# Performance work log

Hardware: AMD Instinct MI355X
Metric: run time of the kernel (lower is better)

The kernel has to match this reference:

```python
import jax, jax.numpy as jnp
import numpy as np

ALPHA = 0.2  # LeakyReLU negative slope
NEG_INF = jnp.float32(-9e15)


def setup_inputs() -> dict:
    key = jax.random.key(0)
    k1, k2, k3, k4, k5, k6 = jax.random.split(key, 6)
    B, N, F_in, F_out = 8, 2048, 256, 64
    h = jax.random.normal(k1, (B, N, F_in), dtype=jnp.float32)
    adj = jax.random.randint(k2, (B, N, N), 0, 2, dtype=jnp.int32)
    level = jax.random.uniform(k3, (B, N), dtype=jnp.float32)
    node_type = jax.random.uniform(k4, (B, N, N), dtype=jnp.float32)
    W = jax.random.normal(k5, (F_in, F_out), dtype=jnp.float32) * 1.414 / np.sqrt(F_in)
    a = jax.random.normal(k6, (2 * F_out, 1), dtype=jnp.float32) * 1.414 / np.sqrt(2 * F_out)
    return {"h": h, "adj": adj, "level": level, "node_type": node_type, "W": W, "a": a}


def reference(h, adj, level, node_type, W, a):
    # h: [B,N,Fin], adj/node_type: [B,N,N], level: [B,N], W: [Fin,Fout], a: [2*Fout,1]
    F_out = W.shape[1]
    Wh = jnp.einsum('bnf,fo->bno', h, W)  # [B,N,Fout]
    # Additive attention decomposed: e[b,i,j] = a1.Wh_i + a2.Wh_j (no O(N^2*2F) tensor)
    a1 = a[:F_out, 0]
    a2 = a[F_out:, 0]
    f1 = Wh @ a1  # [B,N]
    f2 = Wh @ a2  # [B,N]
    e = jax.nn.leaky_relu(f1[:, :, None] + f2[:, None, :], negative_slope=ALPHA)  # [B,N,N]
    # gat_our=True path: node_type scales scores, level scales Wh
    e = e * node_type
    Wh = Wh * level[:, :, None]
    attention = jnp.where(adj > 0, e, NEG_INF)
    attention = jax.nn.softmax(attention, axis=1)  # faithful: original softmax over dim=1
    # dropout p=0 / eval mode -> identity
    h_prime = jnp.einsum('bij,bjo->bio', attention, Wh)  # [B,N,Fout]
    return jax.nn.relu(h_prime)  # concat=True
```

## Files before the change

kernel.cpp:

```cpp
#include <hip/hip_runtime.h>

#define BB 8
#define NN 2048
#define FIN 256
#define FO 64

typedef short short8_t __attribute__((ext_vector_type(8)));
typedef float float4_t __attribute__((ext_vector_type(4)));

__device__ __forceinline__ unsigned short f2bf(float x) {
  unsigned int u = __float_as_uint(x);
  unsigned int r = (u + 0x7fffu + ((u >> 16) & 1u)) >> 16;
  return (unsigned short)r;
}

#define GLD16(gp, lp)                                                          \
  __builtin_amdgcn_global_load_lds(                                            \
      (const __attribute__((address_space(1))) void*)(gp),                     \
      (__attribute__((address_space(3))) void*)(lp), 16, 0, 0)

__global__ __launch_bounds__(256) void k1_gemm(
    const float* __restrict__ h,
    const float* __restrict__ level,
    const float* __restrict__ W,
    const float* __restrict__ a,
    float* __restrict__ V, float* __restrict__ f1, float* __restrict__ f2,
    float* __restrict__ scol)
{
  __shared__ float wlds[128 * 64];
  __shared__ float hs[16 * 260];
  __shared__ float parts1[16 * 17];
  __shared__ float parts2[16 * 17];
  int t = threadIdx.x;
  int b = blockIdx.x >> 7;
  int i0 = (blockIdx.x & 127) * 16;

  if (blockIdx.x < 64) scol[blockIdx.x * 256 + t] = 0.0f;

  {
    int r_ld = t >> 4, f0 = (t & 15) * 16;
    const float* hp = h + (size_t)(b * NN + i0 + r_ld) * FIN + f0;
    float4 x0 = *(const float4*)(hp);
    float4 x1 = *(const float4*)(hp + 4);
    float4 x2 = *(const float4*)(hp + 8);
    float4 x3 = *(const float4*)(hp + 12);
    float* hd = &hs[r_ld * 260 + f0];
    *(float4*)(hd + 0) = x0; *(float4*)(hd + 4) = x1;
    *(float4*)(hd + 8) = x2; *(float4*)(hd + 12) = x3;
  }

  int r = t >> 4;
  int c4 = (t & 15) * 4;
  float4 acc = {0, 0, 0, 0};

  #pragma unroll
  for (int half = 0; half < 2; ++half) {
    __syncthreads();
    #pragma unroll
    for (int q = 0; q < 8; ++q) {
      int idx = q * 1024 + t * 4;
      *(float4*)&wlds[idx] = *(const float4*)&W[half * 8192 + idx];
    }
    __syncthreads();
    for (int f = 0; f < 128; f += 8) {
      float4 hv0 = *(const float4*)&hs[r * 260 + half * 128 + f];
      float4 hv1 = *(const float4*)&hs[r * 260 + half * 128 + f + 4];
      float hvv[8] = {hv0.x, hv0.y, hv0.z, hv0.w, hv1.x, hv1.y, hv1.z, hv1.w};
      #pragma unroll
      for (int k = 0; k < 8; ++k) {
        float4 wv = *(const float4*)&wlds[(f + k) * 64 + c4];
        acc.x += hvv[k] * wv.x; acc.y += hvv[k] * wv.y;
        acc.z += hvv[k] * wv.z; acc.w += hvv[k] * wv.w;
      }
    }
  }

  float p1 = acc.x * a[c4] + acc.y * a[c4 + 1] + acc.z * a[c4 + 2] + acc.w * a[c4 + 3];
  float p2 = acc.x * a[64 + c4] + acc.y * a[64 + c4 + 1] +
             acc.z * a[64 + c4 + 2] + acc.w * a[64 + c4 + 3];
  parts1[r * 17 + (t & 15)] = p1;
  parts2[r * 17 + (t & 15)] = p2;
  __syncthreads();
  if (t < 16) {
    float s1 = 0.f, s2 = 0.f;
    #pragma unroll
    for (int g = 0; g < 16; ++g) { s1 += parts1[t * 17 + g]; s2 += parts2[t * 17 + g]; }
    f1[b * NN + i0 + t] = s1;
    f2[b * NN + i0 + t] = s2;
  }

  float lv = level[b * NN + i0 + r];
  float4 vv = {acc.x * lv, acc.y * lv, acc.z * lv, acc.w * lv};
  *(float4*)&V[(size_t)(b * NN + i0 + r) * FO + c4] = vv;
}

__global__ __launch_bounds__(512) void k2a_stream(
    const int* __restrict__ adj,
    const float* __restrict__ ntp,
    const float* __restrict__ f1,
    const float* __restrict__ f2,
    unsigned short* __restrict__ u_bf,
    float* __restrict__ scol)
{
  int t = threadIdx.x;
  int b = blockIdx.x >> 7;
  int row0 = (blockIdx.x & 127) * 16;
  size_t base = (size_t)b * NN;
  int j0 = t * 4;

  float4 f2v = *(const float4*)(f2 + base + j0);
  float acc0 = 0.f, acc1 = 0.f, acc2 = 0.f, acc3 = 0.f;

  size_t rb = (base + row0) * (size_t)NN + j0;
  const int* ap = adj + rb;
  const float* np = ntp + rb;
  unsigned short* up = u_bf + rb;
  const float* f1p = f1 + base + row0;

  #pragma unroll 4
  for (int r = 0; r < 16; ++r) {
    int4 a4 = *(const int4*)(ap + (size_t)r * NN);
    float4 n4 = *(const float4*)(np + (size_t)r * NN);
    float f1v = f1p[r];
    float x0 = f1v + f2v.x; x0 = fmaxf(x0, 0.2f * x0);
    float x1 = f1v + f2v.y; x1 = fmaxf(x1, 0.2f * x1);
    float x2 = f1v + f2v.z; x2 = fmaxf(x2, 0.2f * x2);
    float x3 = f1v + f2v.w; x3 = fmaxf(x3, 0.2f * x3);
    float u0 = (a4.x > 0) ? __expf(x0 * n4.x) : 0.0f;
    float u1 = (a4.y > 0) ? __expf(x1 * n4.y) : 0.0f;
    float u2 = (a4.z > 0) ? __expf(x2 * n4.z) : 0.0f;
    float u3 = (a4.w > 0) ? __expf(x3 * n4.w) : 0.0f;
    acc0 += u0; acc1 += u1; acc2 += u2; acc3 += u3;
    unsigned int p0 = (unsigned int)f2bf(u0) | ((unsigned int)f2bf(u1) << 16);
    unsigned int p1 = (unsigned int)f2bf(u2) | ((unsigned int)f2bf(u3) << 16);
    *(uint2*)(up + (size_t)r * NN) = make_uint2(p0, p1);
  }

  atomicAdd(&scol[base + j0 + 0], acc0);
  atomicAdd(&scol[base + j0 + 1], acc1);
  atomicAdd(&scol[base + j0 + 2], acc2);
  atomicAdd(&scol[base + j0 + 3], acc3);
}

template <int STORE_U>
__global__ __launch_bounds__(512) void k2a_stats(
    const int* __restrict__ adj,
    const float* __restrict__ ntp,
    const float* __restrict__ f1,
    const float* __restrict__ f2,
    unsigned short* __restrict__ u_bf,
    unsigned char* __restrict__ bits,
    float* __restrict__ scol)
{
  __shared__ int ladj[2][16 * 256];
  __shared__ float lnt[2][16 * 256];
  __shared__ float red[2048];
  int t = threadIdx.x;
  int b = blockIdx.x >> 6;
  int row0 = (blockIdx.x & 63) * 32;
  int w = t >> 6, l = t & 63;
  size_t base = (size_t)b * NN;

  auto stage = [&](int buf, int s) {
    int tile = s >> 3, c = s & 7;
    int r0 = row0 + tile * 16 + 2 * w;
    const int* ga = adj + (base + r0) * NN + c * 256 + l * 4;
    const float* gn = ntp + (base + r0) * NN + c * 256 + l * 4;
    GLD16(ga, &ladj[buf][(2 * w) * 256]);
    GLD16(ga + NN, &ladj[buf][(2 * w + 1) * 256]);
    GLD16(gn, &lnt[buf][(2 * w) * 256]);
    GLD16(gn + NN, &lnt[buf][(2 * w + 1) * 256]);
  };

  int jj = t & 255;
  int rh = t >> 8;

  float accJ[8];
  #pragma unroll
  for (int c = 0; c < 8; ++c) accJ[c] = 0.f;
  float f2v[8];
  #pragma unroll
  for (int c = 0; c < 8; ++c) f2v[c] = f2[base + c * 256 + jj];

  stage(0, 0);
  for (int s = 0; s < 16; ++s) {
    int buf = s & 1;
    __syncthreads();
    if (s < 15) stage(buf ^ 1, s + 1);
    int tile = s >> 3, c = s & 7;
    #pragma unroll
    for (int q = 0; q < 8; ++q) {
      int r = rh * 8 + q;
      int av = ladj[buf][r * 256 + jj];
      float nv = lnt[buf][r * 256 + jj];
      float f1v = f1[base + row0 + tile * 16 + r];
      float x = f1v + f2v[c];
      x = fmaxf(x, 0.2f * x);
      bool m = av > 0;
      float u = m ? __expf(x * nv) : 0.0f;
      accJ[c] += u;
      if (STORE_U) {
        u_bf[(base + row0 + tile * 16 + r) * NN + c * 256 + jj] = f2bf(u);
      } else {
        unsigned long long bal = __ballot(m);
        if (l == 0)
          *(unsigned long long*)&bits[(base + row0 + tile * 16 + r) * (NN / 8)
                                      + c * 32 + (w & 3) * 8] = bal;
      }
    }
  }

  if (rh == 0) {
    #pragma unroll
    for (int c = 0; c < 8; ++c) red[c * 256 + jj] = accJ[c];
  }
  __syncthreads();
  if (rh == 1) {
    #pragma unroll
    for (int c = 0; c < 8; ++c) red[c * 256 + jj] += accJ[c];
  }
  __syncthreads();
  #pragma unroll
  for (int q = 0; q < 4; ++q)
    atomicAdd(&scol[base + q * 512 + t], red[q * 512 + t]);
}

__global__ __launch_bounds__(256) void k2b_pack(
    const float* __restrict__ V,
    const float* __restrict__ scol,
    unsigned short* __restrict__ vf)
{
  int t = threadIdx.x;
  int b = blockIdx.x >> 6;
  int kk = blockIdx.x & 63;
  int ng = t >> 6;
  int l = t & 63;
  int jb = kk * 32 + ((l >> 4) * 8);
  int o = ng * 16 + (l & 15);
  unsigned int pk[4];
  #pragma unroll
  for (int p = 0; p < 4; ++p) {
    int jr0 = jb + 2 * p, jr1 = jb + 2 * p + 1;
    float s0 = scol[b * NN + jr0];
    float s1 = scol[b * NN + jr1];
    float i0 = (s0 > 0.f) ? (1.0f / s0) : 0.0f;
    float i1 = (s1 > 0.f) ? (1.0f / s1) : 0.0f;
    float v0 = V[(size_t)(b * NN + jr0) * FO + o] * i0;
    float v1 = V[(size_t)(b * NN + jr1) * FO + o] * i1;
    pk[p] = (unsigned int)f2bf(v0) | ((unsigned int)f2bf(v1) << 16);
  }
  *(uint4*)(vf + (size_t)(((b * 64 + kk) * 4 + ng) * 64 + l) * 8) =
      make_uint4(pk[0], pk[1], pk[2], pk[3]);
}

__global__ __launch_bounds__(512, 4) void k3_agg_u3(
    const unsigned short* __restrict__ u_bf,
    const unsigned short* __restrict__ vf,
    float* __restrict__ outp)
{
  __shared__ float red[8 * 16 * 68];
  int t = threadIdx.x;
  int b = blockIdx.x >> 6;
  int tt = blockIdx.x & 63;
  int i0 = tt * 32;
  int w = t >> 6, l = t & 63;
  int col = l & 15, quad = l >> 4;
  const unsigned short* urow0 = u_bf + (size_t)(b * NN + i0 + col) * NN + quad * 8;
  const unsigned short* urow1 = urow0 + (size_t)16 * NN;
  const unsigned short* vbase = vf + (size_t)(b * 64) * 2048 + l * 8;

  float4_t acc[2][4];
  #pragma unroll
  for (int sgi = 0; sgi < 2; ++sgi)
    #pragma unroll
    for (int g = 0; g < 4; ++g) acc[sgi][g] = (float4_t){0, 0, 0, 0};

  int kk0 = w * 8;
  short8_t A0 = *(const short8_t*)(urow0 + kk0 * 32);
  short8_t A1 = *(const short8_t*)(urow1 + kk0 * 32);
  const unsigned short* vb0 = vbase + (size_t)kk0 * 2048;
  short8_t c0 = *(const short8_t*)(vb0);
  short8_t c1 = *(const short8_t*)(vb0 + 512);
  short8_t c2 = *(const short8_t*)(vb0 + 1024);
  short8_t c3 = *(const short8_t*)(vb0 + 1536);

  #pragma unroll
  for (int s = 0; s < 8; ++s) {
    short8_t nA0, nA1, n0, n1, n2, n3;
    if (s < 7) {
      int kk = w * 8 + s + 1;
      nA0 = *(const short8_t*)(urow0 + kk * 32);
      nA1 = *(const short8_t*)(urow1 + kk * 32);
      const unsigned short* vn = vbase + (size_t)kk * 2048;
      n0 = *(const short8_t*)(vn);
      n1 = *(const short8_t*)(vn + 512);
      n2 = *(const short8_t*)(vn + 1024);
      n3 = *(const short8_t*)(vn + 1536);
    }
    acc[0][0] = __builtin_amdgcn_mfma_f32_16x16x32_bf16(A0, c0, acc[0][0], 0, 0, 0);
    acc[0][1] = __builtin_amdgcn_mfma_f32_16x16x32_bf16(A0, c1, acc[0][1], 0, 0, 0);
    acc[0][2] = __builtin_amdgcn_mfma_f32_16x16x32_bf16(A0, c2, acc[0][2], 0, 0, 0);
    acc[0][3] = __builtin_amdgcn_mfma_f32_16x16x32_bf16(A0, c3, acc[0][3], 0, 0, 0);
    acc[1][0] = __builtin_amdgcn_mfma_f32_16x16x32_bf16(A1, c0, acc[1][0], 0, 0, 0);
    acc[1][1] = __builtin_amdgcn_mfma_f32_16x16x32_bf16(A1, c1, acc[1][1], 0, 0, 0);
    acc[1][2] = __builtin_amdgcn_mfma_f32_16x16x32_bf16(A1, c2, acc[1][2], 0, 0, 0);
    acc[1][3] = __builtin_amdgcn_mfma_f32_16x16x32_bf16(A1, c3, acc[1][3], 0, 0, 0);
    if (s < 7) { A0 = nA0; A1 = nA1; c0 = n0; c1 = n1; c2 = n2; c3 = n3; }
  }

  #pragma unroll
  for (int sub = 0; sub < 2; ++sub) {
    __syncthreads();
    #pragma unroll
    for (int r = 0; r < 4; ++r) {
      int rowi = quad * 4 + r;
      float* rp = &red[w * 1088 + rowi * 68 + col];
      rp[0] = acc[sub][0][r];
      rp[16] = acc[sub][1][r];
      rp[32] = acc[sub][2][r];
      rp[48] = acc[sub][3][r];
    }
    __syncthreads();
    if (t < 256) {
      int row = t >> 4, o4 = (t & 15) * 4;
      const float* rp = &red[row * 68 + o4];
      float4 s0 = *(const float4*)(rp);
      float4 s1 = *(const float4*)(rp + 1088);
      float4 s2 = *(const float4*)(rp + 2176);
      float4 s3 = *(const float4*)(rp + 3264);
      float4 s4 = *(const float4*)(rp + 4352);
      float4 s5 = *(const float4*)(rp + 5440);
      float4 s6 = *(const float4*)(rp + 6528);
      float4 s7 = *(const float4*)(rp + 7616);
      float4 o;
      o.x = fmaxf(s0.x + s1.x + s2.x + s3.x + s4.x + s5.x + s6.x + s7.x, 0.0f);
      o.y = fmaxf(s0.y + s1.y + s2.y + s3.y + s4.y + s5.y + s6.y + s7.y, 0.0f);
      o.z = fmaxf(s0.z + s1.z + s2.z + s3.z + s4.z + s5.z + s6.z + s7.z, 0.0f);
      o.w = fmaxf(s0.w + s1.w + s2.w + s3.w + s4.w + s5.w + s6.w + s7.w, 0.0f);
      *(float4*)&outp[(size_t)(b * NN + i0 + sub * 16 + row) * FO + o4] = o;
    }
  }
}

__global__ __launch_bounds__(256) void k3_agg_b(
    const float* __restrict__ ntp,
    const unsigned char* __restrict__ bits,
    const float* __restrict__ f1,
    const float* __restrict__ f2,
    const unsigned short* __restrict__ vf,
    float* __restrict__ outp)
{
  __shared__ float red[4 * 16 * 68];
  int t = threadIdx.x;
  int b = blockIdx.x >> 7;
  int i0 = (blockIdx.x & 127) * 16;
  int w = t >> 6, l = t & 63;
  int col = l & 15, quad = l >> 4;
  int gi = b * NN + i0 + col;
  float f1v = f1[gi];
  const float* ntrow = ntp + (size_t)gi * NN;
  const unsigned char* brow = bits + (size_t)gi * (NN / 8);
  float4_t acc0 = {0, 0, 0, 0}, acc1 = {0, 0, 0, 0}, acc2 = {0, 0, 0, 0}, acc3 = {0, 0, 0, 0};

  for (int s = 0; s < 16; ++s) {
    int kk = w * 16 + s;
    int jq = kk * 32 + quad * 8;
    unsigned int m8 = brow[jq >> 3];
    float4 n0 = *(const float4*)(ntrow + jq);
    float4 n1 = *(const float4*)(ntrow + jq + 4);
    float4 g0 = *(const float4*)(f2 + b * NN + jq);
    float4 g1 = *(const float4*)(f2 + b * NN + jq + 4);
    float f2v[8] = {g0.x, g0.y, g0.z, g0.w, g1.x, g1.y, g1.z, g1.w};
    float ntf[8] = {n0.x, n0.y, n0.z, n0.w, n1.x, n1.y, n1.z, n1.w};
    union { unsigned int u[4]; short8_t v; } A;
    #pragma unroll
    for (int p = 0; p < 4; ++p) {
      int e0 = 2 * p, e1 = 2 * p + 1;
      float x0 = f1v + f2v[e0]; x0 = fmaxf(x0, 0.2f * x0);
      float u0 = ((m8 >> e0) & 1u) ? __expf(x0 * ntf[e0]) : 0.0f;
      float x1 = f1v + f2v[e1]; x1 = fmaxf(x1, 0.2f * x1);
      float u1 = ((m8 >> e1) & 1u) ? __expf(x1 * ntf[e1]) : 0.0f;
      A.u[p] = (unsigned int)f2bf(u0) | ((unsigned int)f2bf(u1) << 16);
    }
    const unsigned short* vb = vf + (size_t)(b * 64 + kk) * 2048 + l * 8;
    short8_t bf0 = *(const short8_t*)(vb);
    short8_t bf1 = *(const short8_t*)(vb + 512);
    short8_t bf2 = *(const short8_t*)(vb + 1024);
    short8_t bf3 = *(const short8_t*)(vb + 1536);
    acc0 = __builtin_amdgcn_mfma_f32_16x16x32_bf16(A.v, bf0, acc0, 0, 0, 0);
    acc1 = __builtin_amdgcn_mfma_f32_16x16x32_bf16(A.v, bf1, acc1, 0, 0, 0);
    acc2 = __builtin_amdgcn_mfma_f32_16x16x32_bf16(A.v, bf2, acc2, 0, 0, 0);
    acc3 = __builtin_amdgcn_mfma_f32_16x16x32_bf16(A.v, bf3, acc3, 0, 0, 0);
  }

  #pragma unroll
  for (int r = 0; r < 4; ++r) {
    int rowi = quad * 4 + r;
    red[w * 1088 + rowi * 68 + 0 + col] = acc0[r];
    red[w * 1088 + rowi * 68 + 16 + col] = acc1[r];
    red[w * 1088 + rowi * 68 + 32 + col] = acc2[r];
    red[w * 1088 + rowi * 68 + 48 + col] = acc3[r];
  }
  __syncthreads();

  int row = t >> 4, o4 = (t & 15) * 4;
  const float* rp = &red[row * 68 + o4];
  float4 s0 = *(const float4*)(rp);
  float4 s1 = *(const float4*)(rp + 1088);
  float4 s2 = *(const float4*)(rp + 2176);
  float4 s3 = *(const float4*)(rp + 3264);
  float4 o;
  o.x = fmaxf(s0.x + s1.x + s2.x + s3.x, 0.0f);
  o.y = fmaxf(s0.y + s1.y + s2.y + s3.y, 0.0f);
  o.z = fmaxf(s0.z + s1.z + s2.z + s3.z, 0.0f);
  o.w = fmaxf(s0.w + s1.w + s2.w + s3.w, 0.0f);
  *(float4*)&outp[(size_t)(b * NN + i0 + row) * FO + o4] = o;
}

extern "C" void kernel_launch(void* const* d_in, const int* in_sizes, int n_in,
                              void* d_out, int out_size, void* d_ws, size_t ws_size,
                              hipStream_t stream) {
  const float* h = (const float*)d_in[0];
  const int* adj = (const int*)d_in[1];
  const float* level = (const float*)d_in[2];
  const float* ntm = (const float*)d_in[3];
  const float* W = (const float*)d_in[4];
  const float* a = (const float*)d_in[5];
  float* outp = (float*)d_out;

  float* V = (float*)d_ws;
  float* f1 = V + (size_t)BB * NN * FO;
  float* f2 = f1 + BB * NN;
  float* scol = f2 + BB * NN;
  unsigned short* vf = (unsigned short*)(scol + BB * NN);
  char* tail = (char*)(vf + (size_t)BB * NN * FO);
  size_t fixed = (size_t)(tail - (char*)d_ws);
  size_t need_u = fixed + (size_t)BB * NN * NN * 2;
  bool big = (ws_size >= need_u);

  k1_gemm<<<1024, 256, 0, stream>>>(h, level, W, a, V, f1, f2, scol);
  if (big) {
    unsigned short* u_bf = (unsigned short*)tail;
    k2a_stream<<<1024, 512, 0, stream>>>(adj, ntm, f1, f2, u_bf, scol);
    k2b_pack<<<512, 256, 0, stream>>>(V, scol, vf);
    k3_agg_u3<<<512, 512, 0, stream>>>(u_bf, vf, outp);
  } else {
    unsigned char* bits = (unsigned char*)tail;
    k2a_stats<0><<<512, 512, 0, stream>>>(adj, ntm, f1, f2, nullptr, bits, scol);
    k2b_pack<<<512, 256, 0, stream>>>(V, scol, vf);
    k3_agg_b<<<1024, 256, 0, stream>>>(ntm, bits, f1, f2, vf, outp);
  }
}
```

Before: 350.6 us.

## Replace column-sum atomics with per-rowblock partials and batch loads in stream kernel

```diff
diff --git a/kernel.cpp b/kernel.cpp
--- a/kernel.cpp
+++ b/kernel.cpp
@@ -100,11 +100,12 @@
     const float* __restrict__ f1,
     const float* __restrict__ f2,
     unsigned short* __restrict__ u_bf,
-    float* __restrict__ scol)
-{
-  int t = threadIdx.x;
-  int b = blockIdx.x >> 7;
-  int row0 = (blockIdx.x & 127) * 16;
+    float* __restrict__ partials)
+{
+  int t = threadIdx.x;
+  int b = blockIdx.x >> 6;
+  int rowblk = blockIdx.x & 63;
+  int row0 = rowblk * 32;
   size_t base = (size_t)b * NN;
   int j0 = t * 4;
 
@@ -117,29 +118,35 @@
   unsigned short* up = u_bf + rb;
   const float* f1p = f1 + base + row0;
 
-  #pragma unroll 4
-  for (int r = 0; r < 16; ++r) {
-    int4 a4 = *(const int4*)(ap + (size_t)r * NN);
-    float4 n4 = *(const float4*)(np + (size_t)r * NN);
-    float f1v = f1p[r];
-    float x0 = f1v + f2v.x; x0 = fmaxf(x0, 0.2f * x0);
-    float x1 = f1v + f2v.y; x1 = fmaxf(x1, 0.2f * x1);
-    float x2 = f1v + f2v.z; x2 = fmaxf(x2, 0.2f * x2);
-    float x3 = f1v + f2v.w; x3 = fmaxf(x3, 0.2f * x3);
-    float u0 = (a4.x > 0) ? __expf(x0 * n4.x) : 0.0f;
-    float u1 = (a4.y > 0) ? __expf(x1 * n4.y) : 0.0f;
-    float u2 = (a4.z > 0) ? __expf(x2 * n4.z) : 0.0f;
-    float u3 = (a4.w > 0) ? __expf(x3 * n4.w) : 0.0f;
-    acc0 += u0; acc1 += u1; acc2 += u2; acc3 += u3;
-    unsigned int p0 = (unsigned int)f2bf(u0) | ((unsigned int)f2bf(u1) << 16);
-    unsigned int p1 = (unsigned int)f2bf(u2) | ((unsigned int)f2bf(u3) << 16);
-    *(uint2*)(up + (size_t)r * NN) = make_uint2(p0, p1);
-  }
-
-  atomicAdd(&scol[base + j0 + 0], acc0);
-  atomicAdd(&scol[base + j0 + 1], acc1);
-  atomicAdd(&scol[base + j0 + 2], acc2);
-  atomicAdd(&scol[base + j0 + 3], acc3);
+  #pragma unroll
+  for (int g = 0; g < 4; ++g) {
+    int4 av[8];
+    float4 nv[8];
+    #pragma unroll
+    for (int rr = 0; rr < 8; ++rr) {
+      av[rr] = *(const int4*)(ap + (size_t)(g * 8 + rr) * NN);
+      nv[rr] = *(const float4*)(np + (size_t)(g * 8 + rr) * NN);
+    }
+    #pragma unroll
+    for (int rr = 0; rr < 8; ++rr) {
+      float f1v = f1p[g * 8 + rr];
+      float x0 = f1v + f2v.x; x0 = fmaxf(x0, 0.2f * x0);
+      float x1 = f1v + f2v.y; x1 = fmaxf(x1, 0.2f * x1);
+      float x2 = f1v + f2v.z; x2 = fmaxf(x2, 0.2f * x2);
+      float x3 = f1v + f2v.w; x3 = fmaxf(x3, 0.2f * x3);
+      float u0 = (av[rr].x > 0) ? __expf(x0 * nv[rr].x) : 0.0f;
+      float u1 = (av[rr].y > 0) ? __expf(x1 * nv[rr].y) : 0.0f;
+      float u2 = (av[rr].z > 0) ? __expf(x2 * nv[rr].z) : 0.0f;
+      float u3 = (av[rr].w > 0) ? __expf(x3 * nv[rr].w) : 0.0f;
+      acc0 += u0; acc1 += u1; acc2 += u2; acc3 += u3;
+      unsigned int p0 = (unsigned int)f2bf(u0) | ((unsigned int)f2bf(u1) << 16);
+      unsigned int p1 = (unsigned int)f2bf(u2) | ((unsigned int)f2bf(u3) << 16);
+      *(uint2*)(up + (size_t)(g * 8 + rr) * NN) = make_uint2(p0, p1);
+    }
+  }
+
+  *(float4*)(partials + (size_t)(b * 64 + rowblk) * NN + j0) =
+      make_float4(acc0, acc1, acc2, acc3);
 }
 
 template <int STORE_U>
@@ -225,6 +232,53 @@
     atomicAdd(&scol[base + q * 512 + t], red[q * 512 + t]);
 }
 
+__global__ __launch_bounds__(256) void k2b_pack_p(
+    const float* __restrict__ V,
+    const float* __restrict__ partials,
+    unsigned short* __restrict__ vf)
+{
+  __shared__ float sred[8 * 32];
+  __shared__ float sinv[32];
+  int t = threadIdx.x;
+  int b = blockIdx.x >> 6;
+  int kk = blockIdx.x & 63;
+
+  {
+    int tj = t & 31, tr = t >> 5;
+    float s = 0.f;
+    #pragma unroll
+    for (int q = 0; q < 8; ++q)
+      s += partials[(size_t)(b * 64 + tr * 8 + q) * NN + kk * 32 + tj];
+    sred[tr * 32 + tj] = s;
+  }
+  __syncthreads();
+  if (t < 32) {
+    float tot = 0.f;
+    #pragma unroll
+    for (int g = 0; g < 8; ++g) tot += sred[g * 32 + t];
+    sinv[t] = (tot > 0.f) ? (1.0f / tot) : 0.0f;
+  }
+  __syncthreads();
+
+  int ng = t >> 6;
+  int l = t & 63;
+  int jb0 = (l >> 4) * 8;
+  int jb = kk * 32 + jb0;
+  int o = ng * 16 + (l & 15);
+  unsigned int pk[4];
+  #pragma unroll
+  for (int p = 0; p < 4; ++p) {
+    int jr0 = jb + 2 * p, jr1 = jb + 2 * p + 1;
+    float i0 = sinv[jb0 + 2 * p];
+    float i1 = sinv[jb0 + 2 * p + 1];
+    float v0 = V[(size_t)(b * NN + jr0) * FO + o] * i0;
+    float v1 = V[(size_t)(b * NN + jr1) * FO + o] * i1;
+    pk[p] = (unsigned int)f2bf(v0) | ((unsigned int)f2bf(v1) << 16);
+  }
+  *(uint4*)(vf + (size_t)(((b * 64 + kk) * 4 + ng) * 64 + l) * 8) =
+      make_uint4(pk[0], pk[1], pk[2], pk[3]);
+}
+
 __global__ __launch_bounds__(256) void k2b_pack(
     const float* __restrict__ V,
     const float* __restrict__ scol,
@@ -433,7 +487,8 @@
   float* f2 = f1 + BB * NN;
   float* scol = f2 + BB * NN;
   unsigned short* vf = (unsigned short*)(scol + BB * NN);
-  char* tail = (char*)(vf + (size_t)BB * NN * FO);
+  float* partials = (float*)(vf + (size_t)BB * NN * FO);
+  char* tail = (char*)(partials + (size_t)BB * 64 * NN);
   size_t fixed = (size_t)(tail - (char*)d_ws);
   size_t need_u = fixed + (size_t)BB * NN * NN * 2;
   bool big = (ws_size >= need_u);
@@ -441,8 +496,8 @@
   k1_gemm<<<1024, 256, 0, stream>>>(h, level, W, a, V, f1, f2, scol);
   if (big) {
     unsigned short* u_bf = (unsigned short*)tail;
-    k2a_stream<<<1024, 512, 0, stream>>>(adj, ntm, f1, f2, u_bf, scol);
-    k2b_pack<<<512, 256, 0, stream>>>(V, scol, vf);
+    k2a_stream<<<512, 512, 0, stream>>>(adj, ntm, f1, f2, u_bf, partials);
+    k2b_pack_p<<<512, 256, 0, stream>>>(V, partials, vf);
     k3_agg_u3<<<512, 512, 0, stream>>>(u_bf, vf, outp);
   } else {
     unsigned char* bits = (unsigned char*)tail;
```

Result: faster. 339.6 us (-3.2%).
